# Kernel optimization log

Measured on AMD Instinct MI355X. Metric: run time of the kernel, lower is better.

Reference implementation:

```python
import jax, jax.numpy as jnp
import numpy as np

B, T, E, H = 128, 256, 256, 256


def setup_inputs() -> dict:
    key = jax.random.key(0)
    ks = jax.random.split(key, 8)
    s = 1.0 / np.sqrt(H)
    x = jax.random.normal(ks[0], (B, T, E), jnp.float32)
    # valid shift-reduce sequence: [S] + [S,R]*(T-1) -> T shifts, T-1 reduces
    trans = np.zeros((2 * T - 1, B), np.int32)
    trans[2::2, :] = 1
    u = lambda k, shp: jax.random.uniform(k, shp, jnp.float32, -s, s)
    return {
        "x": x,
        "transitions": jnp.asarray(trans),
        "Wx": u(ks[1], (H, E)), "bx": u(ks[2], (H,)),
        "Wg": u(ks[3], (H, E)), "bg": u(ks[4], (H,)),
        "Wr": u(ks[5], (5 * H, 2 * H)), "br": u(ks[6], (5 * H,)),
    }


def reference(x, transitions, Wx, bx, Wg, bg, Wr, br):
    Bb, Tt, _ = x.shape
    Hh = Wx.shape[0]
    # buffers: c = proj_x(x), h = sigmoid(proj_x_gate(x)) * tanh(c)
    c_buf = jnp.einsum("bte,he->bth", x, Wx) + bx
    h_buf = jax.nn.sigmoid(jnp.einsum("bte,he->bth", x, Wg) + bg) * jnp.tanh(c_buf)
    buffers = jnp.concatenate([h_buf, c_buf], axis=-1)  # [B, T, 2H]
    bidx = jnp.arange(Bb)

    def cell(left, right):
        # left/right: [B, 2H] = (h, c) pairs
        hl, cl = jnp.split(left, 2, axis=-1)
        hr, cr = jnp.split(right, 2, axis=-1)
        proj = jnp.concatenate([hl, hr], axis=-1) @ Wr.T + br  # [B, 5H]
        i, fl, fr, g, o = jnp.split(proj, 5, axis=-1)
        c = (jax.nn.sigmoid(fl) * cl + jax.nn.sigmoid(fr) * cr
             + jax.nn.sigmoid(i) * jnp.tanh(g))
        h = jax.nn.sigmoid(o) * jnp.tanh(c)
        return jnp.concatenate([h, c], axis=-1)

    def step(carry, tr):
        stack, sp, bp = carry  # stack [B,T,2H], pointers [B] int32
        is_shift = tr == 0
        shift_val = buffers[bidx, jnp.maximum(bp - 1, 0)]       # buffer.pop()
        left = stack[bidx, jnp.maximum(sp - 2, 0)]
        right = stack[bidx, jnp.maximum(sp - 1, 0)]
        reduced = cell(left, right)
        new_val = jnp.where(is_shift[:, None], shift_val, reduced)
        new_sp = jnp.where(is_shift, sp + 1, sp - 1)
        stack = stack.at[bidx, new_sp - 1].set(new_val)
        new_bp = jnp.where(is_shift, bp - 1, bp)
        return (stack, new_sp, new_bp), None

    init = (jnp.zeros((Bb, Tt, 2 * Hh), x.dtype),
            jnp.zeros((Bb,), jnp.int32),
            jnp.full((Bb,), Tt, jnp.int32))
    (stack, sp, _), _ = jax.lax.scan(step, init, transitions)
    # root state: h half of top of stack
    return stack[bidx, sp - 1][:, :Hh]
```

## Files before the change

kernel.cpp:

```cpp
#include <hip/hip_runtime.h>

typedef short bf16x8 __attribute__((ext_vector_type(8)));
typedef float f32x4 __attribute__((ext_vector_type(4)));
typedef unsigned int u32;
typedef unsigned short u16;

#define B_ 128
#define T_ 256
#define E_ 256
#define H_ 256

__device__ __forceinline__ u16 f2bf(float f){
  u32 x = __float_as_uint(f);
  x += 0x7FFFu + ((x >> 16) & 1u);
  return (u16)(x >> 16);
}
__device__ __forceinline__ float sigf(float x){ return 1.0f/(1.0f + __expf(-x)); }
__device__ __forceinline__ float tanhf_(float x){ return 2.0f/(1.0f + __expf(-2.0f*x)) - 1.0f; }

__global__ void cvt4(const float* __restrict__ s, u16* __restrict__ d, int n4){
  int i = blockIdx.x*blockDim.x + threadIdx.x;
  int st = gridDim.x*blockDim.x;
  for (; i < n4; i += st){
    float4 f = ((const float4*)s)[i];
    ushort4 o;
    o.x=f2bf(f.x); o.y=f2bf(f.y); o.z=f2bf(f.z); o.w=f2bf(f.w);
    ((ushort4*)d)[i] = o;
  }
}

__global__ __launch_bounds__(256) void leaf_kernel(
    const u16* __restrict__ xb, const u16* __restrict__ wxb, const u16* __restrict__ wgb,
    const float* __restrict__ bx, const float* __restrict__ bg,
    float* __restrict__ c_buf, u16* __restrict__ h_buf){
  int wid  = (blockIdx.x << 2) | (threadIdx.x >> 6);
  int lane = threadIdx.x & 63;
  int mt = wid >> 4, nt = wid & 15;
  int m0 = mt << 4, h0 = nt << 4;
  int lr = lane & 15, lg = lane >> 4;
  f32x4 accC = {0,0,0,0}, accG = {0,0,0,0};
  int arow = (m0 + lr) * E_;
  int wrow = (h0 + lr) * E_;
  #pragma unroll
  for (int c = 0; c < 8; ++c){
    int kb = c*32 + lg*8;
    bf16x8 af = *(const bf16x8*)(xb  + arow + kb);
    bf16x8 wx = *(const bf16x8*)(wxb + wrow + kb);
    bf16x8 wg = *(const bf16x8*)(wgb + wrow + kb);
    accC = __builtin_amdgcn_mfma_f32_16x16x32_bf16(af, wx, accC, 0,0,0);
    accG = __builtin_amdgcn_mfma_f32_16x16x32_bf16(af, wg, accG, 0,0,0);
  }
  int h = h0 + lr;
  float bxv = bx[h], bgv = bg[h];
  #pragma unroll
  for (int q = 0; q < 4; ++q){
    int m = m0 + lg*4 + q;
    float cv = accC[q] + bxv;
    float hv = sigf(accG[q] + bgv) * tanhf_(cv);
    c_buf[m*H_ + h] = cv;
    h_buf[m*H_ + h] = f2bf(hv);
  }
}

__global__ __launch_bounds__(320) void tree_kernel(
    const float* __restrict__ Wr, const float* __restrict__ br,
    const float* __restrict__ c_buf, const u16* __restrict__ h_buf,
    u32* __restrict__ h_tag, float* __restrict__ out){
  __shared__ __align__(16) char A[16384];
  __shared__ float proj[5*256];
  int tid  = threadIdx.x;
  int wave = tid >> 6, lane = tid & 63;
  int lr = lane & 15, lg = lane >> 4;
  int bi = blockIdx.x & 7, ji = blockIdx.x >> 3;
  int b0 = bi << 4, j0 = ji << 4;

  bf16x8 wfrag[16];
  {
    const float* wp = Wr + (wave*H_ + j0 + lr) * (2*H_);
    #pragma unroll
    for (int c = 0; c < 16; ++c){
      const float4* p = (const float4*)(wp + c*32 + lg*8);
      float4 u = p[0], v = p[1];
      bf16x8 w;
      w[0]=(short)f2bf(u.x); w[1]=(short)f2bf(u.y); w[2]=(short)f2bf(u.z); w[3]=(short)f2bf(u.w);
      w[4]=(short)f2bf(v.x); w[5]=(short)f2bf(v.y); w[6]=(short)f2bf(v.z); w[7]=(short)f2bf(v.w);
      wfrag[c] = w;
    }
  }

  float c_state = 0.f, brv0=0.f, brv1=0.f, brv2=0.f, brv3=0.f, brv4=0.f;
  int b_ = 0, j_ = 0;
  if (tid < 256){
    b_ = b0 + (tid >> 4); j_ = j0 + (tid & 15);
    brv0 = br[0*H_ + j_]; brv1 = br[1*H_ + j_]; brv2 = br[2*H_ + j_];
    brv3 = br[3*H_ + j_]; brv4 = br[4*H_ + j_];
    c_state = c_buf[(b_*T_ + 255)*H_ + j_];
  }

  for (int r = 0; r < 255; ++r){
    int idx = 254 - r;
    float c_leaf = 0.f;
    if (tid < 256) c_leaf = c_buf[(b_*T_ + idx)*H_ + j_];

    if (tid < 256){
      if (r == 0){
        #pragma unroll
        for (int i = 0; i < 16; ++i){
          u16 v = h_buf[((b0+i)*T_ + 255)*H_ + tid];
          int off = i*1024 + tid*2;
          *(short*)&A[off ^ ((i&7)<<4)] = (short)v;
        }
      } else {
        const u32* spn = h_tag + ((r-1)&1)*32768 + b0*H_ + tid;
        u32 v[16];
        #pragma unroll
        for (int i = 0; i < 16; ++i)
          v[i] = __hip_atomic_load(spn + i*H_, __ATOMIC_RELAXED, __HIP_MEMORY_SCOPE_AGENT);
        u32 want = ((u32)r) << 16;
        #pragma unroll
        for (int i = 0; i < 16; ++i){
          while ((v[i] & 0xFFFF0000u) != want){
            __builtin_amdgcn_s_sleep(1);
            v[i] = __hip_atomic_load(spn + i*H_, __ATOMIC_RELAXED, __HIP_MEMORY_SCOPE_AGENT);
          }
        }
        #pragma unroll
        for (int i = 0; i < 16; ++i){
          int off = i*1024 + tid*2;
          *(short*)&A[off ^ ((i&7)<<4)] = (short)(v[i] & 0xFFFFu);
        }
      }
    } else {
      int l = tid - 256;
      #pragma unroll
      for (int q2 = 0; q2 < 8; ++q2){
        int chunk = q2*64 + l;
        int row = chunk >> 5, qq = chunk & 31;
        bf16x8 v = *(const bf16x8*)(h_buf + ((b0+row)*T_ + idx)*H_ + qq*8);
        int off = row*1024 + 512 + qq*16;
        *(bf16x8*)&A[off ^ ((row&7)<<4)] = v;
      }
    }
    __syncthreads();

    f32x4 acc = {0,0,0,0};
    #pragma unroll
    for (int c = 0; c < 16; ++c){
      int off = lr*1024 + c*64 + lg*16;
      bf16x8 af = *(const bf16x8*)&A[off ^ ((lr&7)<<4)];
      acc = __builtin_amdgcn_mfma_f32_16x16x32_bf16(af, wfrag[c], acc, 0,0,0);
    }
    #pragma unroll
    for (int q = 0; q < 4; ++q)
      proj[wave*256 + (lg*4+q)*16 + lr] = acc[q];
    __syncthreads();

    if (tid < 256){
      float iv = proj[        tid] + brv0;
      float fl = proj[256  + tid] + brv1;
      float fr = proj[512  + tid] + brv2;
      float gv = proj[768  + tid] + brv3;
      float ov = proj[1024 + tid] + brv4;
      float cn = sigf(fl)*c_state + sigf(fr)*c_leaf + sigf(iv)*tanhf_(gv);
      float hn = sigf(ov)*tanhf_(cn);
      c_state = cn;
      if (r == 254){
        out[b_*H_ + j_] = hn;
      } else {
        u32 w = (((u32)(r+1)) << 16) | (u32)f2bf(hn);
        __hip_atomic_store(h_tag + (r&1)*32768 + b_*H_ + j_, w,
                           __ATOMIC_RELAXED, __HIP_MEMORY_SCOPE_AGENT);
      }
    }
  }
}

extern "C" void kernel_launch(void* const* d_in, const int* in_sizes, int n_in,
                              void* d_out, int out_size, void* d_ws, size_t ws_size,
                              hipStream_t stream){
  const float* x  = (const float*)d_in[0];
  const float* Wx = (const float*)d_in[2];
  const float* bx = (const float*)d_in[3];
  const float* Wg = (const float*)d_in[4];
  const float* bg = (const float*)d_in[5];
  const float* Wr = (const float*)d_in[6];
  const float* br = (const float*)d_in[7];
  float* out = (float*)d_out;

  char* ws = (char*)d_ws;
  u16*   xb    = (u16*)(ws);
  u16*   wxb   = (u16*)(ws + 16777216);
  u16*   wgb   = (u16*)(ws + 16908288);
  u16*   h_buf = (u16*)(ws + 17039360);
  float* c_buf = (float*)(ws + 33816576);
  u32*   h_tag = (u32*)(ws + 67371008);

  cvt4<<<2048, 256, 0, stream>>>(x,  xb,  8388608/4);
  cvt4<<<64,   256, 0, stream>>>(Wx, wxb, 65536/4);
  cvt4<<<64,   256, 0, stream>>>(Wg, wgb, 65536/4);
  leaf_kernel<<<8192, 256, 0, stream>>>(xb, wxb, wgb, bx, bg, c_buf, h_buf);
  hipMemsetAsync(h_tag, 0, 262144, stream);
  tree_kernel<<<128, 320, 0, stream>>>(Wr, br, c_buf, h_buf, h_tag, out);
}
```

Measured before the change: 1.010 ms.

## Double-buffer leaf tiles and overlap leaf MFMAs with cross-block state wait

Splits the shared A tile into a stack-state part and a double-buffered leaf part. The extra wave prefetches the next step's leaf h rows into registers and stores them to the alternate buffer, and the leaf half of the MFMA reduction is issued before the inter-block spin-wait. Each compute thread now loads 16 contiguous tagged words and packs them into two 16-byte LDS stores. The spin loop polls all words together and drops the s_sleep. The aim is to take leaf loads and half the MFMA work off the serial critical path. In exchange it uses more LDS and registers, and busy-polling without sleep can add memory traffic.

After: 921.2 us. 1.1x faster.

```diff
diff --git a/kernel.cpp b/kernel.cpp
--- a/kernel.cpp
+++ b/kernel.cpp
@@ -66,13 +66,14 @@
     const float* __restrict__ Wr, const float* __restrict__ br,
     const float* __restrict__ c_buf, const u16* __restrict__ h_buf,
     u32* __restrict__ h_tag, float* __restrict__ out){
-  __shared__ __align__(16) char A[16384];
+  __shared__ __align__(16) char Sst[8192];
+  __shared__ __align__(16) char Slf[2][8192];
   __shared__ float proj[5*256];
-  int tid  = threadIdx.x;
-  int wave = tid >> 6, lane = tid & 63;
-  int lr = lane & 15, lg = lane >> 4;
-  int bi = blockIdx.x & 7, ji = blockIdx.x >> 3;
-  int b0 = bi << 4, j0 = ji << 4;
+  const int tid  = threadIdx.x;
+  const int wave = tid >> 6, lane = tid & 63;
+  const int lr = lane & 15, lg = lane >> 4;
+  const int bi = blockIdx.x & 7, ji = blockIdx.x >> 3;
+  const int b0 = bi << 4, j0 = ji << 4;
 
   bf16x8 wfrag[16];
   {
@@ -88,66 +89,102 @@
     }
   }
 
-  float c_state = 0.f, brv0=0.f, brv1=0.f, brv2=0.f, brv3=0.f, brv4=0.f;
-  int b_ = 0, j_ = 0;
-  if (tid < 256){
-    b_ = b0 + (tid >> 4); j_ = j0 + (tid & 15);
-    brv0 = br[0*H_ + j_]; brv1 = br[1*H_ + j_]; brv2 = br[2*H_ + j_];
-    brv3 = br[3*H_ + j_]; brv4 = br[4*H_ + j_];
+  const bool isC = (tid < 256);
+  const int pb = tid >> 4, pj = tid & 15;
+  const int b_ = b0 + pb, j_ = j0 + pj;
+
+  float brv0=0.f, brv1=0.f, brv2=0.f, brv3=0.f, brv4=0.f;
+  float c_state = 0.f, c_leaf = 0.f;
+  if (isC){
+    brv0 = br[j_]; brv1 = br[H_+j_]; brv2 = br[2*H_+j_];
+    brv3 = br[3*H_+j_]; brv4 = br[4*H_+j_];
     c_state = c_buf[(b_*T_ + 255)*H_ + j_];
   }
 
+  if (isC){
+    const u16* hp = h_buf + (b_*T_ + 255)*H_ + pj*16;
+    bf16x8 a = *(const bf16x8*)hp;
+    bf16x8 b = *(const bf16x8*)(hp + 8);
+    int base = pb*512 + pj*32, swz = (pb&7)<<4;
+    *(bf16x8*)&Sst[(base     ) ^ swz] = a;
+    *(bf16x8*)&Sst[(base + 16) ^ swz] = b;
+  } else {
+    int l = tid - 256;
+    #pragma unroll
+    for (int q = 0; q < 8; ++q){
+      int chunk = q*64 + l;
+      int row = chunk >> 5, col = chunk & 31;
+      bf16x8 v = *(const bf16x8*)(h_buf + ((b0+row)*T_ + 254)*H_ + col*8);
+      *(bf16x8*)&Slf[0][(row*512 + col*16) ^ ((row&7)<<4)] = v;
+    }
+  }
+  __syncthreads();
+
   for (int r = 0; r < 255; ++r){
-    int idx = 254 - r;
-    float c_leaf = 0.f;
-    if (tid < 256) c_leaf = c_buf[(b_*T_ + idx)*H_ + j_];
-
-    if (tid < 256){
-      if (r == 0){
+    if (isC) c_leaf = c_buf[(b_*T_ + (254-r))*H_ + j_];
+
+    bf16x8 lf[8];
+    if (!isC && r < 254){
+      int l = tid - 256, idxn = 253 - r;
+      #pragma unroll
+      for (int q = 0; q < 8; ++q){
+        int chunk = q*64 + l;
+        int row = chunk >> 5, col = chunk & 31;
+        lf[q] = *(const bf16x8*)(h_buf + ((b0+row)*T_ + idxn)*H_ + col*8);
+      }
+    }
+
+    u32 v[16];
+    const u32* sp = h_tag + ((r-1)&1)*32768 + b_*256 + pj*16;
+    if (isC && r){
+      #pragma unroll
+      for (int i = 0; i < 16; ++i)
+        v[i] = __hip_atomic_load(sp+i, __ATOMIC_RELAXED, __HIP_MEMORY_SCOPE_AGENT);
+    }
+
+    f32x4 acc = {0,0,0,0};
+    #pragma unroll
+    for (int c = 8; c < 16; ++c){
+      int off = (lr*512 + (c-8)*64 + lg*16) ^ ((lr&7)<<4);
+      bf16x8 af = *(const bf16x8*)&Slf[r&1][off];
+      acc = __builtin_amdgcn_mfma_f32_16x16x32_bf16(af, wfrag[c], acc, 0,0,0);
+    }
+
+    if (isC && r){
+      const u32 want = ((u32)r) << 16;
+      for (;;){
+        u32 m = 0;
         #pragma unroll
-        for (int i = 0; i < 16; ++i){
-          u16 v = h_buf[((b0+i)*T_ + 255)*H_ + tid];
-          int off = i*1024 + tid*2;
-          *(short*)&A[off ^ ((i&7)<<4)] = (short)v;
-        }
-      } else {
-        const u32* spn = h_tag + ((r-1)&1)*32768 + b0*H_ + tid;
-        u32 v[16];
+        for (int i = 0; i < 16; ++i) m |= (v[i] ^ want);
+        if (!(m & 0xFFFF0000u)) break;
         #pragma unroll
         for (int i = 0; i < 16; ++i)
-          v[i] = __hip_atomic_load(spn + i*H_, __ATOMIC_RELAXED, __HIP_MEMORY_SCOPE_AGENT);
-        u32 want = ((u32)r) << 16;
-        #pragma unroll
-        for (int i = 0; i < 16; ++i){
-          while ((v[i] & 0xFFFF0000u) != want){
-            __builtin_amdgcn_s_sleep(1);
-            v[i] = __hip_atomic_load(spn + i*H_, __ATOMIC_RELAXED, __HIP_MEMORY_SCOPE_AGENT);
-          }
-        }
-        #pragma unroll
-        for (int i = 0; i < 16; ++i){
-          int off = i*1024 + tid*2;
-          *(short*)&A[off ^ ((i&7)<<4)] = (short)(v[i] & 0xFFFFu);
-        }
-      }
-    } else {
+          v[i] = __hip_atomic_load(sp+i, __ATOMIC_RELAXED, __HIP_MEMORY_SCOPE_AGENT);
+      }
+      uint4 qa, qb;
+      qa.x = (v[0]&0xFFFFu)|(v[1]<<16);  qa.y = (v[2]&0xFFFFu)|(v[3]<<16);
+      qa.z = (v[4]&0xFFFFu)|(v[5]<<16);  qa.w = (v[6]&0xFFFFu)|(v[7]<<16);
+      qb.x = (v[8]&0xFFFFu)|(v[9]<<16);  qb.y = (v[10]&0xFFFFu)|(v[11]<<16);
+      qb.z = (v[12]&0xFFFFu)|(v[13]<<16); qb.w = (v[14]&0xFFFFu)|(v[15]<<16);
+      int base = pb*512 + pj*32, swz = (pb&7)<<4;
+      *(uint4*)&Sst[(base     ) ^ swz] = qa;
+      *(uint4*)&Sst[(base + 16) ^ swz] = qb;
+    }
+    if (!isC && r < 254){
       int l = tid - 256;
       #pragma unroll
-      for (int q2 = 0; q2 < 8; ++q2){
-        int chunk = q2*64 + l;
-        int row = chunk >> 5, qq = chunk & 31;
-        bf16x8 v = *(const bf16x8*)(h_buf + ((b0+row)*T_ + idx)*H_ + qq*8);
-        int off = row*1024 + 512 + qq*16;
-        *(bf16x8*)&A[off ^ ((row&7)<<4)] = v;
+      for (int q = 0; q < 8; ++q){
+        int chunk = q*64 + l;
+        int row = chunk >> 5, col = chunk & 31;
+        *(bf16x8*)&Slf[(r+1)&1][(row*512 + col*16) ^ ((row&7)<<4)] = lf[q];
       }
     }
     __syncthreads();
 
-    f32x4 acc = {0,0,0,0};
-    #pragma unroll
-    for (int c = 0; c < 16; ++c){
-      int off = lr*1024 + c*64 + lg*16;
-      bf16x8 af = *(const bf16x8*)&A[off ^ ((lr&7)<<4)];
+    #pragma unroll
+    for (int c = 0; c < 8; ++c){
+      int off = (lr*512 + c*64 + lg*16) ^ ((lr&7)<<4);
+      bf16x8 af = *(const bf16x8*)&Sst[off];
       acc = __builtin_amdgcn_mfma_f32_16x16x32_bf16(af, wfrag[c], acc, 0,0,0);
     }
     #pragma unroll
@@ -155,7 +192,7 @@
       proj[wave*256 + (lg*4+q)*16 + lr] = acc[q];
     __syncthreads();
 
-    if (tid < 256){
+    if (isC){
       float iv = proj[        tid] + brv0;
       float fl = proj[256  + tid] + brv1;
       float fr = proj[512  + tid] + brv2;
@@ -163,14 +200,14 @@
       float ov = proj[1024 + tid] + brv4;
       float cn = sigf(fl)*c_state + sigf(fr)*c_leaf + sigf(iv)*tanhf_(gv);
       float hn = sigf(ov)*tanhf_(cn);
+      if (r < 254){
+        u32 w = (((u32)(r+1)) << 16) | (u32)f2bf(hn);
+        __hip_atomic_store(h_tag + (r&1)*32768 + b_*256 + j_, w,
+                           __ATOMIC_RELAXED, __HIP_MEMORY_SCOPE_AGENT);
+      } else {
+        out[b_*H_ + j_] = hn;
+      }
       c_state = cn;
-      if (r == 254){
-        out[b_*H_ + j_] = hn;
-      } else {
-        u32 w = (((u32)(r+1)) << 16) | (u32)f2bf(hn);
-        __hip_atomic_store(h_tag + (r&1)*32768 + b_*H_ + j_, w,
-                           __ATOMIC_RELAXED, __HIP_MEMORY_SCOPE_AGENT);
-      }
     }
   }
 }
```

## Precompute right-child projection off the serial chain and split tree across block pairs

Applied to the files above, without the earlier changes.

The right-child (leaf) half of the recurrent projection does not depend on the recurrence, so it is now computed for all steps up front in a separate parallel kernel (projL, bf16, bias folded in). Only the left-state half of the matmul stays on the serial chain. The tree kernel is reorganised into 16 blocks, each pairing with a partner block over half the hidden dimension. Each block computes its own half's contribution before waiting on the partner's h values, which overlaps the flag polling with MFMA work. This shortens the per-step critical path and reduces cross-block synchronisation fan-in. The cost is an extra kernel, extra workspace, and additional bf16 rounding of the leaf projection.

Measured after the change: 3.169 ms. 3.14x slower.

```diff
diff --git a/kernel.cpp b/kernel.cpp
--- a/kernel.cpp
+++ b/kernel.cpp
@@ -10,11 +10,15 @@
 #define E_ 256
 #define H_ 256
 
+#define AL(p) __hip_atomic_load((p), __ATOMIC_RELAXED, __HIP_MEMORY_SCOPE_AGENT)
+#define AS(p,v) __hip_atomic_store((p), (v), __ATOMIC_RELAXED, __HIP_MEMORY_SCOPE_AGENT)
+
 __device__ __forceinline__ u16 f2bf(float f){
   u32 x = __float_as_uint(f);
   x += 0x7FFFu + ((x >> 16) & 1u);
   return (u16)(x >> 16);
 }
+__device__ __forceinline__ float bf2f(u16 v){ return __uint_as_float(((u32)v) << 16); }
 __device__ __forceinline__ float sigf(float x){ return 1.0f/(1.0f + __expf(-x)); }
 __device__ __forceinline__ float tanhf_(float x){ return 2.0f/(1.0f + __expf(-2.0f*x)) - 1.0f; }
 
@@ -62,116 +66,162 @@
   }
 }
 
-__global__ __launch_bounds__(320) void tree_kernel(
-    const float* __restrict__ Wr, const float* __restrict__ br,
-    const float* __restrict__ c_buf, const u16* __restrict__ h_buf,
+__global__ __launch_bounds__(256) void projl2_kernel(
+    const u16* __restrict__ wrb, const float* __restrict__ br,
+    const u16* __restrict__ h_buf, u16* __restrict__ projL){
+  int wv = threadIdx.x >> 6, lane = threadIdx.x & 63;
+  int lr = lane & 15, lg = lane >> 4;
+  int id = blockIdx.x*4 + wv;
+  int bt = id & 7, gj = id >> 3;
+  int g = gj >> 4, j16 = gj & 15;
+  bf16x8 af[8];
+  {
+    const u16* wp = wrb + (u32)(g*256 + j16*16 + lr)*512 + 256 + lg*8;
+    #pragma unroll
+    for (int c = 0; c < 8; ++c) af[c] = *(const bf16x8*)(wp + c*32);
+  }
+  float bias[4];
+  #pragma unroll
+  for (int q = 0; q < 4; ++q) bias[q] = br[g*256 + j16*16 + lg*4 + q];
+  const u16* hb = h_buf + ((u32)(bt*16 + lr)*T_)*H_ + lg*8;
+
+  for (int i = 0; i < 128; ++i){
+    int r0 = i, r1 = i + 128;
+    bool ok1 = (r1 < 255);
+    int t0 = 254 - r0, t1 = 254 - r1;
+    bf16x8 b0[8], b1[8];
+    #pragma unroll
+    for (int c = 0; c < 8; ++c) b0[c] = *(const bf16x8*)(hb + t0*H_ + c*32);
+    if (ok1){
+      #pragma unroll
+      for (int c = 0; c < 8; ++c) b1[c] = *(const bf16x8*)(hb + t1*H_ + c*32);
+    }
+    f32x4 a0, a1;
+    #pragma unroll
+    for (int q = 0; q < 4; ++q){ a0[q] = bias[q]; a1[q] = bias[q]; }
+    #pragma unroll
+    for (int c = 0; c < 8; ++c){
+      a0 = __builtin_amdgcn_mfma_f32_16x16x32_bf16(af[c], b0[c], a0, 0,0,0);
+      if (ok1) a1 = __builtin_amdgcn_mfma_f32_16x16x32_bf16(af[c], b1[c], a1, 0,0,0);
+    }
+    #pragma unroll
+    for (int q = 0; q < 4; ++q){
+      u32 grow = (u32)(g*256 + j16*16 + lg*4 + q);
+      projL[(((u32)r0*8 + bt)*1280 + grow)*16 + lr] = f2bf(a0[q]);
+      if (ok1) projL[(((u32)r1*8 + bt)*1280 + grow)*16 + lr] = f2bf(a1[q]);
+    }
+  }
+}
+
+__global__ __launch_bounds__(512, 2) void tree3_kernel(
+    const u16* __restrict__ wrb, const float* __restrict__ c_buf,
+    const u16* __restrict__ h_buf, const u16* __restrict__ projL,
     u32* __restrict__ h_tag, float* __restrict__ out){
-  __shared__ __align__(16) char A[16384];
-  __shared__ float proj[5*256];
-  int tid  = threadIdx.x;
-  int wave = tid >> 6, lane = tid & 63;
-  int lr = lane & 15, lg = lane >> 4;
-  int bi = blockIdx.x & 7, ji = blockIdx.x >> 3;
-  int b0 = bi << 4, j0 = ji << 4;
-
-  bf16x8 wfrag[16];
+  __shared__ __align__(16) char Sst[8192];
+  const int tid = threadIdx.x;
+  const int wv = tid >> 6, lane = tid & 63;
+  const int lr = lane & 15, lg = lane >> 4;
+  const int pr = blockIdx.x & 7, hf = blockIdx.x >> 3;
+  const int b0 = pr << 4;
+  const int jb = hf << 7, pjb = jb ^ 128;
+  const int jg = jb + wv*16 + lr;
+  const int cb = hf << 2;
+
+  bf16x8 wf[5][8];
+  #pragma unroll
+  for (int g = 0; g < 5; ++g){
+    const u16* wp = wrb + (u32)(g*256 + jg)*512 + lg*8;
+    #pragma unroll
+    for (int c = 0; c < 8; ++c) wf[g][c] = *(const bf16x8*)(wp + c*32);
+  }
+
+  float cst[4];
+  #pragma unroll
+  for (int q = 0; q < 4; ++q)
+    cst[q] = c_buf[((b0 + lg*4 + q)*T_ + 255)*H_ + jg];
+
   {
-    const float* wp = Wr + (wave*H_ + j0 + lr) * (2*H_);
-    #pragma unroll
-    for (int c = 0; c < 16; ++c){
-      const float4* p = (const float4*)(wp + c*32 + lg*8);
-      float4 u = p[0], v = p[1];
-      bf16x8 w;
-      w[0]=(short)f2bf(u.x); w[1]=(short)f2bf(u.y); w[2]=(short)f2bf(u.z); w[3]=(short)f2bf(u.w);
-      w[4]=(short)f2bf(v.x); w[5]=(short)f2bf(v.y); w[6]=(short)f2bf(v.z); w[7]=(short)f2bf(v.w);
-      wfrag[c] = w;
-    }
-  }
-
-  float c_state = 0.f, brv0=0.f, brv1=0.f, brv2=0.f, brv3=0.f, brv4=0.f;
-  int b_ = 0, j_ = 0;
-  if (tid < 256){
-    b_ = b0 + (tid >> 4); j_ = j0 + (tid & 15);
-    brv0 = br[0*H_ + j_]; brv1 = br[1*H_ + j_]; brv2 = br[2*H_ + j_];
-    brv3 = br[3*H_ + j_]; brv4 = br[4*H_ + j_];
-    c_state = c_buf[(b_*T_ + 255)*H_ + j_];
-  }
+    int bl = tid >> 5, cq = tid & 31;
+    bf16x8 v = *(const bf16x8*)(h_buf + ((b0+bl)*T_ + 255)*H_ + cq*8);
+    *(bf16x8*)&Sst[((bl<<9) + (cq<<4)) ^ ((bl&7)<<4)] = v;
+  }
+  ushort4 pf[5];
+  #pragma unroll
+  for (int g = 0; g < 5; ++g)
+    pf[g] = *(const ushort4*)(projL + (((u32)0*8 + pr)*1280 + g*256 + jg)*16 + lg*4);
+  __syncthreads();
+
+  const int blp = tid >> 5, jqp = tid & 31;
 
   for (int r = 0; r < 255; ++r){
-    int idx = 254 - r;
-    float c_leaf = 0.f;
-    if (tid < 256) c_leaf = c_buf[(b_*T_ + idx)*H_ + j_];
-
-    if (tid < 256){
-      if (r == 0){
-        #pragma unroll
-        for (int i = 0; i < 16; ++i){
-          u16 v = h_buf[((b0+i)*T_ + 255)*H_ + tid];
-          int off = i*1024 + tid*2;
-          *(short*)&A[off ^ ((i&7)<<4)] = (short)v;
-        }
+    float clf[4];
+    #pragma unroll
+    for (int q = 0; q < 4; ++q)
+      clf[q] = c_buf[((b0 + lg*4 + q)*T_ + (254-r))*H_ + jg];
+
+    u32 v0=0,v1=0,v2=0,v3=0;
+    const u32* sp = h_tag + ((r-1)&1)*32768 + ((b0+blp)<<8) + pjb + (jqp<<2);
+    if (r){ v0=AL(sp); v1=AL(sp+1); v2=AL(sp+2); v3=AL(sp+3); }
+
+    f32x4 acc[5];
+    #pragma unroll
+    for (int g = 0; g < 5; ++g){
+      acc[g][0]=bf2f(pf[g].x); acc[g][1]=bf2f(pf[g].y);
+      acc[g][2]=bf2f(pf[g].z); acc[g][3]=bf2f(pf[g].w);
+    }
+    if (r < 254){
+      #pragma unroll
+      for (int g = 0; g < 5; ++g)
+        pf[g] = *(const ushort4*)(projL + (((u32)(r+1)*8 + pr)*1280 + g*256 + jg)*16 + lg*4);
+    }
+
+    #pragma unroll
+    for (int c = 0; c < 4; ++c){
+      int off = ((lr<<9) + ((cb+c)<<6) + (lg<<4)) ^ ((lr&7)<<4);
+      bf16x8 a = *(const bf16x8*)&Sst[off];
+      #pragma unroll
+      for (int g = 0; g < 5; ++g)
+        acc[g] = __builtin_amdgcn_mfma_f32_16x16x32_bf16(a, wf[g][cb+c], acc[g], 0,0,0);
+    }
+
+    if (r){
+      const u32 want = ((u32)r) << 16;
+      while ((((v0^want)|(v1^want)|(v2^want)|(v3^want)) >> 16) != 0u){
+        v0=AL(sp); v1=AL(sp+1); v2=AL(sp+2); v3=AL(sp+3);
+      }
+      uint2 pk;
+      pk.x = (v0 & 0xFFFFu) | (v1 << 16);
+      pk.y = (v2 & 0xFFFFu) | (v3 << 16);
+      *(uint2*)&Sst[((blp<<9) + ((pjb + (jqp<<2))<<1)) ^ ((blp&7)<<4)] = pk;
+    }
+    __syncthreads();
+
+    #pragma unroll
+    for (int c = 0; c < 4; ++c){
+      int cc = (cb ^ 4) + c;
+      int off = ((lr<<9) + (cc<<6) + (lg<<4)) ^ ((lr&7)<<4);
+      bf16x8 a = *(const bf16x8*)&Sst[off];
+      #pragma unroll
+      for (int g = 0; g < 5; ++g)
+        acc[g] = __builtin_amdgcn_mfma_f32_16x16x32_bf16(a, wf[g][cc], acc[g], 0,0,0);
+    }
+
+    #pragma unroll
+    for (int q = 0; q < 4; ++q){
+      float iv = acc[0][q], fl = acc[1][q], fr = acc[2][q];
+      float gv = acc[3][q], ov = acc[4][q];
+      float cn = sigf(fl)*cst[q] + sigf(fr)*clf[q] + sigf(iv)*tanhf_(gv);
+      float hn = sigf(ov)*tanhf_(cn);
+      cst[q] = cn;
+      if (r < 254){
+        AS(h_tag + (r&1)*32768 + ((b0+lg*4+q)<<8) + jg,
+           (((u32)(r+1)) << 16) | (u32)f2bf(hn));
+        *(u16*)&Sst[(((lg*4+q)<<9) + (jg<<1)) ^ (((lg*4+q)&7)<<4)] = f2bf(hn);
       } else {
-        const u32* spn = h_tag + ((r-1)&1)*32768 + b0*H_ + tid;
-        u32 v[16];
-        #pragma unroll
-        for (int i = 0; i < 16; ++i)
-          v[i] = __hip_atomic_load(spn + i*H_, __ATOMIC_RELAXED, __HIP_MEMORY_SCOPE_AGENT);
-        u32 want = ((u32)r) << 16;
-        #pragma unroll
-        for (int i = 0; i < 16; ++i){
-          while ((v[i] & 0xFFFF0000u) != want){
-            __builtin_amdgcn_s_sleep(1);
-            v[i] = __hip_atomic_load(spn + i*H_, __ATOMIC_RELAXED, __HIP_MEMORY_SCOPE_AGENT);
-          }
-        }
-        #pragma unroll
-        for (int i = 0; i < 16; ++i){
-          int off = i*1024 + tid*2;
-          *(short*)&A[off ^ ((i&7)<<4)] = (short)(v[i] & 0xFFFFu);
-        }
+        out[(b0+lg*4+q)*H_ + jg] = hn;
       }
-    } else {
-      int l = tid - 256;
-      #pragma unroll
-      for (int q2 = 0; q2 < 8; ++q2){
-        int chunk = q2*64 + l;
-        int row = chunk >> 5, qq = chunk & 31;
-        bf16x8 v = *(const bf16x8*)(h_buf + ((b0+row)*T_ + idx)*H_ + qq*8);
-        int off = row*1024 + 512 + qq*16;
-        *(bf16x8*)&A[off ^ ((row&7)<<4)] = v;
-      }
     }
     __syncthreads();
-
-    f32x4 acc = {0,0,0,0};
-    #pragma unroll
-    for (int c = 0; c < 16; ++c){
-      int off = lr*1024 + c*64 + lg*16;
-      bf16x8 af = *(const bf16x8*)&A[off ^ ((lr&7)<<4)];
-      acc = __builtin_amdgcn_mfma_f32_16x16x32_bf16(af, wfrag[c], acc, 0,0,0);
-    }
-    #pragma unroll
-    for (int q = 0; q < 4; ++q)
-      proj[wave*256 + (lg*4+q)*16 + lr] = acc[q];
-    __syncthreads();
-
-    if (tid < 256){
-      float iv = proj[        tid] + brv0;
-      float fl = proj[256  + tid] + brv1;
-      float fr = proj[512  + tid] + brv2;
-      float gv = proj[768  + tid] + brv3;
-      float ov = proj[1024 + tid] + brv4;
-      float cn = sigf(fl)*c_state + sigf(fr)*c_leaf + sigf(iv)*tanhf_(gv);
-      float hn = sigf(ov)*tanhf_(cn);
-      c_state = cn;
-      if (r == 254){
-        out[b_*H_ + j_] = hn;
-      } else {
-        u32 w = (((u32)(r+1)) << 16) | (u32)f2bf(hn);
-        __hip_atomic_store(h_tag + (r&1)*32768 + b_*H_ + j_, w,
-                           __ATOMIC_RELAXED, __HIP_MEMORY_SCOPE_AGENT);
-      }
-    }
   }
 }
 
@@ -194,11 +244,15 @@
   u16*   h_buf = (u16*)(ws + 17039360);
   float* c_buf = (float*)(ws + 33816576);
   u32*   h_tag = (u32*)(ws + 67371008);
+  u16*   wrb   = (u16*)(ws + 67633152);
+  u16*   projL = (u16*)(ws + 68943872);
 
   cvt4<<<2048, 256, 0, stream>>>(x,  xb,  8388608/4);
   cvt4<<<64,   256, 0, stream>>>(Wx, wxb, 65536/4);
   cvt4<<<64,   256, 0, stream>>>(Wg, wgb, 65536/4);
+  cvt4<<<640,  256, 0, stream>>>(Wr, wrb, 655360/4);
   leaf_kernel<<<8192, 256, 0, stream>>>(xb, wxb, wgb, bx, bg, c_buf, h_buf);
   hipMemsetAsync(h_tag, 0, 262144, stream);
-  tree_kernel<<<128, 320, 0, stream>>>(Wr, br, c_buf, h_buf, h_tag, out);
-}
+  projl2_kernel<<<160, 256, 0, stream>>>(wrb, br, h_buf, projL);
+  tree3_kernel<<<16, 512, 0, stream>>>(wrb, c_buf, h_buf, projL, h_tag, out);
+}
```
